# Kernel optimization log

Measured on AMD Instinct MI355X. Metric: run time of the kernel, lower is better.

The kernel has to match this reference:

```python
import jax, jax.numpy as jnp
import numpy as np

H = 64          # HIDDEN_SIZE
D = 300         # WORD_VEC_DIMS
L = 3           # NUM_LSTM_LAYERS
B = 256
T = 512


def _uniform(key, shape, scale):
    return jax.random.uniform(key, shape, jnp.float32, -scale, scale)


def setup_inputs() -> dict:
    key = jax.random.key(0)
    keys = jax.random.split(key, 32)
    s = 1.0 / np.sqrt(H)  # torch LSTM/Linear init scale
    inp = {
        "input": jax.random.normal(keys[0], (B, T, D), jnp.float32),
        "h_0": jnp.zeros((L, B, H), jnp.float32),
        "c_0": jnp.zeros((L, B, H), jnp.float32),
    }
    k = 1
    for l in range(L):
        din = D if l == 0 else H
        inp[f"wih{l}"] = _uniform(keys[k], (4 * H, din), s); k += 1
        inp[f"whh{l}"] = _uniform(keys[k], (4 * H, H), s); k += 1
        inp[f"bih{l}"] = _uniform(keys[k], (4 * H,), s); k += 1
        inp[f"bhh{l}"] = _uniform(keys[k], (4 * H,), s); k += 1
    inp["w1"] = _uniform(keys[k], (H, H), s); k += 1
    inp["b1"] = _uniform(keys[k], (H,), s); k += 1
    inp["w2"] = _uniform(keys[k], (D, H), s); k += 1
    inp["b2"] = _uniform(keys[k], (D,), s); k += 1
    return inp


def _lstm_layer(x_tbd, h0, c0, Wih, Whh, bih, bhh):
    # x_tbd: [T, B, Din]; precompute input projection outside the scan
    xp = jnp.einsum('tbd,gd->tbg', x_tbd, Wih) + bih  # [T, B, 4H]

    def step(carry, xt):
        h, c = carry
        g = xt + h @ Whh.T + bhh
        i, f, gg, o = jnp.split(g, 4, axis=-1)  # torch gate order: i,f,g,o
        c = jax.nn.sigmoid(f) * c + jax.nn.sigmoid(i) * jnp.tanh(gg)
        h = jax.nn.sigmoid(o) * jnp.tanh(c)
        return (h, c), h

    (hT, cT), hs = jax.lax.scan(step, (h0, c0), xp)
    return hs, hT, cT  # hs: [T, B, H]


def reference(input, h_0, c_0, wih0, whh0, bih0, bhh0, wih1, whh1, bih1, bhh1,
              wih2, whh2, bih2, bhh2, w1, b1, w2, b2):
    wih = [wih0, wih1, wih2]
    whh = [whh0, whh1, whh2]
    bih = [bih0, bih1, bih2]
    bhh = [bhh0, bhh1, bhh2]
    x = jnp.transpose(input, (1, 0, 2))  # [T, B, D]
    hs_n, cs_n = [], []
    for l in range(L):
        x, hT, cT = _lstm_layer(x, h_0[l], c_0[l], wih[l], whh[l], bih[l], bhh[l])
        hs_n.append(hT)
        cs_n.append(cT)
    # x is now [T, B, H] == output.permute(1, 0, 2) of the batch_first LSTM.
    # Faithfully replicate the original permute+view reordering:
    flat = x.reshape(-1, H)                       # time-major flatten
    y = jnp.tanh(flat @ w1.T + b1) @ w2.T + b2    # MLP head
    out = y.reshape(input.shape[0], -1, D)        # reinterpreted batch-major
    h_n = jnp.stack(hs_n)
    c_n = jnp.stack(cs_n)
    return out, h_n, c_n
```

## Files before the change

kernel.cpp:

```cpp
#include <hip/hip_runtime.h>
#include <math.h>


#define TT 512
#define BB 256
#define DD 300
#define HH 64
#define MM (TT * BB)
#define XP 256
#define TC 128
#define NC (TT / TC)

typedef __attribute__((ext_vector_type(8))) short bf16x8;
typedef __attribute__((ext_vector_type(4))) float f32x4;

__device__ __forceinline__ float bf2f(unsigned short u) {
    return __uint_as_float(((unsigned int)u) << 16);
}
__device__ __forceinline__ unsigned short f2bf(float f) {
    unsigned int x = __float_as_uint(f);
    x += 0x7FFFu + ((x >> 16) & 1u);
    return (unsigned short)(x >> 16);
}
__device__ __forceinline__ float tanh_f(float x) { return 1.f - 2.f / (__expf(2.f * x) + 1.f); }

__device__ __forceinline__ float ld1(const void* p, long long i, int md) {
    return md ? ((const float*)p)[i] : bf2f(((const unsigned short*)p)[i]);
}
__device__ __forceinline__ void ld4v(float* d, const void* p, long long i, int md) {
    if (md) {
        float4 v = *(const float4*)((const float*)p + i);
        d[0] = v.x; d[1] = v.y; d[2] = v.z; d[3] = v.w;
    } else {
        ushort4 u = *(const ushort4*)((const unsigned short*)p + i);
        d[0] = bf2f(u.x); d[1] = bf2f(u.y); d[2] = bf2f(u.z); d[3] = bf2f(u.w);
    }
}

__device__ __forceinline__ f32x4 mfma16(bf16x8 a, bf16x8 b, f32x4 c) {
    return __builtin_amdgcn_mfma_f32_16x16x32_bf16(a, b, c, 0, 0, 0);
}

__device__ __forceinline__ f32x4 mfma6(bf16x8 a1, bf16x8 a2, bf16x8 a3,
                                       bf16x8 b1, bf16x8 b2, bf16x8 b3, f32x4 t) {
    t = mfma16(a2, b2, t);
    t = mfma16(a1, b3, t);
    t = mfma16(a3, b1, t);
    t = mfma16(a1, b2, t);
    t = mfma16(a2, b1, t);
    t = mfma16(a1, b1, t);
    return t;
}

__device__ __forceinline__ void split3x4(const float* v, ushort4& h1, ushort4& h2, ushort4& h3) {
    unsigned short a[4], b[4], c[4];
    #pragma unroll
    for (int e = 0; e < 4; ++e) {
        unsigned short x = f2bf(v[e]);
        float r1 = v[e] - bf2f(x);
        unsigned short y = f2bf(r1);
        float r2 = r1 - bf2f(y);
        unsigned short z = f2bf(r2);
        a[e] = x; b[e] = y; c[e] = z;
    }
    h1 = make_ushort4(a[0], a[1], a[2], a[3]);
    h2 = make_ushort4(b[0], b[1], b[2], b[3]);
    h3 = make_ushort4(c[0], c[1], c[2], c[3]);
}

__global__ void detect_kernel(const void* inp, int* mode) {
    if (threadIdx.x == 0 && blockIdx.x == 0) {
        const unsigned short* u = (const unsigned short*)inp;
        int bad = 0;
        for (int i = 0; i < 256; ++i) {
            float f = bf2f(u[i]);
            if (!(f == f) || fabsf(f) > 1e6f) ++bad;
        }
        *mode = (bad >= 4) ? 1 : 0;
    }
}

__global__ __launch_bounds__(256) void init_state(
    const void* h0, const void* c0, float* hstate, float* cstate, const int* modep)
{
    const int md = *modep;
    int i = blockIdx.x * 256 + threadIdx.x;
    if (i < 3 * BB * HH) {
        hstate[i] = ld1(h0, i, md);
        cstate[i] = ld1(c0, i, md);
    }
}

__global__ __launch_bounds__(256) void final_state(
    const float* hstate, const float* cstate, void* out, const int* modep)
{
    const int md = *modep;
    int i = blockIdx.x * 256 + threadIdx.x;
    const long long base = (long long)MM * DD;
    if (i < 3 * BB * HH) {
        if (md) {
            ((float*)out)[base + i] = hstate[i];
            ((float*)out)[base + 3 * BB * HH + i] = cstate[i];
        } else {
            ((unsigned short*)out)[base + i] = f2bf(hstate[i]);
            ((unsigned short*)out)[base + 3 * BB * HH + i] = f2bf(cstate[i]);
        }
    }
}

__global__ __launch_bounds__(256) void split_w(
    const void* __restrict__ src, unsigned short* __restrict__ dst,
    int rsrc, int csrc, int rdst, int cdst, const int* modep)
{
    const int md = *modep;
    int i = blockIdx.x * 256 + threadIdx.x;
    int n = rdst * cdst;
    if (i >= n) return;
    int r = i / cdst, cc = i - r * cdst;
    float v = (r < rsrc && cc < csrc) ? ld1(src, (long long)r * csrc + cc, md) : 0.f;
    unsigned short a = f2bf(v);
    float r1 = v - bf2f(a);
    unsigned short b = f2bf(r1);
    float r2 = r1 - bf2f(b);
    unsigned short c = f2bf(r2);
    dst[i] = a; dst[n + i] = b; dst[2 * n + i] = c;
}

__global__ __launch_bounds__(256, 2) void proj0_chunk(
    const void* __restrict__ inp, const unsigned short* __restrict__ wsp,
    const void* __restrict__ bih, const void* __restrict__ bhh,
    float* __restrict__ xp, const int* modep, int chunk)
{
    const int md = *modep;
    __shared__ __align__(16) unsigned short aS[3][64 * 40];
    __shared__ __align__(16) unsigned short wS[3][256 * 40];
    const int tid = threadIdx.x;
    const int m0 = blockIdx.x * 64;
    const int lane = tid & 63, wv = tid >> 6;
    const int fr = lane & 15, fq = lane >> 4;
    const int ar = tid >> 2, acs = (tid & 3) * 8;
    const int ml = m0 + ar;
    const int b = ml & 255;
    const int t = chunk * TC + (ml >> 8);
    const long long abase = (long long)b * (TT * DD) + (long long)t * DD;
    float bias[4];
    #pragma unroll
    for (int nf = 0; nf < 4; ++nf) {
        int n = wv * 64 + nf * 16 + fr;
        bias[nf] = ld1(bih, n, md) + ld1(bhh, n, md);
    }
    f32x4 acc[4][4] = {};
    for (int p = 0; p < 10; ++p) {
        const int k0 = p * 32;
        #pragma unroll
        for (int q = 0; q < 2; ++q) {
            const int kg = k0 + acs + q * 4;
            float v[4];
            if (kg + 3 < DD) {
                ld4v(v, inp, abase + kg, md);
            } else {
                #pragma unroll
                for (int e = 0; e < 4; ++e)
                    v[e] = (kg + e < DD) ? ld1(inp, abase + kg + e, md) : 0.f;
            }
            ushort4 h1, h2, h3;
            split3x4(v, h1, h2, h3);
            *(ushort4*)(&aS[0][ar * 40 + acs + q * 4]) = h1;
            *(ushort4*)(&aS[1][ar * 40 + acs + q * 4]) = h2;
            *(ushort4*)(&aS[2][ar * 40 + acs + q * 4]) = h3;
        }
        #pragma unroll
        for (int pl = 0; pl < 3; ++pl) {
            const uint4* gw = (const uint4*)(wsp + (size_t)pl * 81920 + (size_t)tid * 320 + k0);
            uint4* dw = (uint4*)(&wS[pl][tid * 40]);
            #pragma unroll
            for (int qq = 0; qq < 4; ++qq) dw[qq] = gw[qq];
        }
        __syncthreads();
        bf16x8 wf[4][3];
        #pragma unroll
        for (int nf = 0; nf < 4; ++nf) {
            #pragma unroll
            for (int pl = 0; pl < 3; ++pl)
                wf[nf][pl] = *(const bf16x8*)(&wS[pl][(wv * 64 + nf * 16 + fr) * 40 + fq * 8]);
        }
        #pragma unroll
        for (int mf = 0; mf < 4; ++mf) {
            bf16x8 a1 = *(const bf16x8*)(&aS[0][(mf * 16 + fr) * 40 + fq * 8]);
            bf16x8 a2 = *(const bf16x8*)(&aS[1][(mf * 16 + fr) * 40 + fq * 8]);
            bf16x8 a3 = *(const bf16x8*)(&aS[2][(mf * 16 + fr) * 40 + fq * 8]);
            #pragma unroll
            for (int nf = 0; nf < 4; ++nf)
                acc[mf][nf] = mfma6(a1, a2, a3, wf[nf][0], wf[nf][1], wf[nf][2], acc[mf][nf]);
        }
        __syncthreads();
    }
    #pragma unroll
    for (int mf = 0; mf < 4; ++mf) {
        #pragma unroll
        for (int nf = 0; nf < 4; ++nf) {
            const int col = wv * 64 + nf * 16 + fr;
            #pragma unroll
            for (int r = 0; r < 4; ++r) {
                const int row = m0 + mf * 16 + fq * 4 + r;
                xp[(long long)row * XP + col] = acc[mf][nf][r] + bias[nf];
            }
        }
    }
}

__global__ __launch_bounds__(256, 2) void projh_chunk(
    const float* __restrict__ A, const unsigned short* __restrict__ wsp,
    const void* __restrict__ bih, const void* __restrict__ bhh,
    float* __restrict__ xp, const int* modep)
{
    const int md = *modep;
    __shared__ __align__(16) unsigned short aS[3][64 * 40];
    __shared__ __align__(16) unsigned short wS[3][256 * 40];
    const int tid = threadIdx.x;
    const int m0 = blockIdx.x * 64;
    const int lane = tid & 63, wv = tid >> 6;
    const int fr = lane & 15, fq = lane >> 4;
    const int ar = tid >> 2, acs = (tid & 3) * 8;
    float bias[4];
    #pragma unroll
    for (int nf = 0; nf < 4; ++nf) {
        int n = wv * 64 + nf * 16 + fr;
        bias[nf] = ld1(bih, n, md) + ld1(bhh, n, md);
    }
    f32x4 acc[4][4] = {};
    #pragma unroll
    for (int p = 0; p < 2; ++p) {
        const int k0 = p * 32;
        #pragma unroll
        for (int q = 0; q < 2; ++q) {
            float v[4];
            const float4 fv = *(const float4*)(A + (long long)(m0 + ar) * HH + k0 + acs + q * 4);
            v[0] = fv.x; v[1] = fv.y; v[2] = fv.z; v[3] = fv.w;
            ushort4 h1, h2, h3;
            split3x4(v, h1, h2, h3);
            *(ushort4*)(&aS[0][ar * 40 + acs + q * 4]) = h1;
            *(ushort4*)(&aS[1][ar * 40 + acs + q * 4]) = h2;
            *(ushort4*)(&aS[2][ar * 40 + acs + q * 4]) = h3;
        }
        #pragma unroll
        for (int pl = 0; pl < 3; ++pl) {
            const uint4* gw = (const uint4*)(wsp + (size_t)pl * 16384 + (size_t)tid * 64 + k0);
            uint4* dw = (uint4*)(&wS[pl][tid * 40]);
            #pragma unroll
            for (int qq = 0; qq < 4; ++qq) dw[qq] = gw[qq];
        }
        __syncthreads();
        bf16x8 wf[4][3];
        #pragma unroll
        for (int nf = 0; nf < 4; ++nf) {
            #pragma unroll
            for (int pl = 0; pl < 3; ++pl)
                wf[nf][pl] = *(const bf16x8*)(&wS[pl][(wv * 64 + nf * 16 + fr) * 40 + fq * 8]);
        }
        #pragma unroll
        for (int mf = 0; mf < 4; ++mf) {
            bf16x8 a1 = *(const bf16x8*)(&aS[0][(mf * 16 + fr) * 40 + fq * 8]);
            bf16x8 a2 = *(const bf16x8*)(&aS[1][(mf * 16 + fr) * 40 + fq * 8]);
            bf16x8 a3 = *(const bf16x8*)(&aS[2][(mf * 16 + fr) * 40 + fq * 8]);
            #pragma unroll
            for (int nf = 0; nf < 4; ++nf)
                acc[mf][nf] = mfma6(a1, a2, a3, wf[nf][0], wf[nf][1], wf[nf][2], acc[mf][nf]);
        }
        __syncthreads();
    }
    #pragma unroll
    for (int mf = 0; mf < 4; ++mf) {
        #pragma unroll
        for (int nf = 0; nf < 4; ++nf) {
            const int col = wv * 64 + nf * 16 + fr;
            #pragma unroll
            for (int r = 0; r < 4; ++r) {
                const int row = m0 + mf * 16 + fq * 4 + r;
                xp[(long long)row * XP + col] = acc[mf][nf][r] + bias[nf];
            }
        }
    }
}

__global__ __launch_bounds__(256) void scan_chunk(
    const float* __restrict__ xp, float* __restrict__ hs,
    const void* __restrict__ whh,
    float* __restrict__ hstate, float* __restrict__ cstate, const int* modep)
{
    const int md = *modep;
    const int b = blockIdx.x;
    const int j = threadIdx.x;
    const int g = ((j & 3) << 6) | (j >> 2);
    const int i = j >> 2;
    const int m = j & 63;
    const int bl = j & 60;
    __shared__ __align__(16) float h_s[2][64];
    float w[64];
    #pragma unroll
    for (int q = 0; q < 16; ++q) {
        float v[4];
        ld4v(v, whh, (long long)g * HH + q * 4, md);
        w[4*q+0]=v[0]; w[4*q+1]=v[1]; w[4*q+2]=v[2]; w[4*q+3]=v[3];
    }
    float c = cstate[b * HH + i];
    h_s[0][m] = hstate[b * HH + m];
    float hval = 0.f;

    const int type = j & 3;
    const float aa = (type == 2) ? 2.f : 1.f;
    const float cc = 1.f - aa;

    const long long xbase = (long long)b * XP + g;
    const long long xstep = (long long)BB * XP;
    float xc[8], xn[8];
    #pragma unroll
    for (int p = 0; p < 8; ++p) xc[p] = xp[xbase + (long long)p * xstep];

    for (int tg = 0; tg < TC; tg += 8) {
        if (tg + 8 < TC) {
            #pragma unroll
            for (int p = 0; p < 8; ++p)
                xn[p] = xp[xbase + (long long)(tg + 8 + p) * xstep];
        }
        #pragma unroll
        for (int u = 0; u < 8; ++u) {
            const int t = tg + u;
            float a0 = xc[u], a1 = 0.f, a2 = 0.f, a3 = 0.f;
            const float4* h4 = (const float4*)h_s[t & 1];
            #pragma unroll
            for (int q = 0; q < 16; ++q) {
                float4 hv = h4[q];
                a0 = fmaf(hv.x, w[4*q+0], a0);
                a1 = fmaf(hv.y, w[4*q+1], a1);
                a2 = fmaf(hv.z, w[4*q+2], a2);
                a3 = fmaf(hv.w, w[4*q+3], a3);
            }
            float gr = (a0 + a1) + (a2 + a3);
            float s = 1.f / (1.f + __expf(-aa * gr));
            float y = fmaf(aa, s, cc);
            float yi = __shfl(y, bl | 0);
            float yf = __shfl(y, bl | 1);
            float yg = __shfl(y, bl | 2);
            float yo = __shfl(y, bl | 3);
            c = yf * c + yi * yg;
            hval = yo * tanh_f(c);
            if ((j & 3) == 0) {
                h_s[(t & 1) ^ 1][i] = hval;
                hs[((long long)t * BB + b) * HH + i] = hval;
            }
            asm volatile("s_waitcnt lgkmcnt(0)\n\ts_barrier" ::: "memory");
        }
        #pragma unroll
        for (int p = 0; p < 8; ++p) xc[p] = xn[p];
    }
    if ((j & 3) == 0) {
        hstate[b * HH + i] = hval;
        cstate[b * HH + i] = c;
    }
}

__global__ __launch_bounds__(256, 1) void head_chunk(
    const float* __restrict__ hs, const unsigned short* __restrict__ w1p,
    const void* __restrict__ b1, const unsigned short* __restrict__ w2p,
    const void* __restrict__ b2, void* __restrict__ out,
    const int* modep, int chunk)
{
    const int md = *modep;
    __shared__ __align__(16) unsigned short aS[3][64 * 72];
    __shared__ __align__(16) unsigned short wS[3][64 * 72];
    __shared__ __align__(16) unsigned short zS[3][64 * 72];
    const int tid = threadIdx.x;
    const int m0 = blockIdx.x * 64;
    const long long gbase = (long long)chunk * TC * BB;
    const int lane = tid & 63, wv = tid >> 6;
    const int fr = lane & 15, fq = lane >> 4;
    const int ar = tid >> 2, cs = (tid & 3) * 16;
    #pragma unroll
    for (int e = 0; e < 4; ++e) {
        float v[4];
        const float4 fv = *(const float4*)(hs + (long long)(m0 + ar) * HH + cs + e * 4);
        v[0] = fv.x; v[1] = fv.y; v[2] = fv.z; v[3] = fv.w;
        ushort4 h1, h2, h3;
        split3x4(v, h1, h2, h3);
        *(ushort4*)(&aS[0][ar * 72 + cs + e * 4]) = h1;
        *(ushort4*)(&aS[1][ar * 72 + cs + e * 4]) = h2;
        *(ushort4*)(&aS[2][ar * 72 + cs + e * 4]) = h3;
    }
    #pragma unroll
    for (int pl = 0; pl < 3; ++pl) {
        const uint4* g1 = (const uint4*)(w1p + (size_t)pl * 4096 + (size_t)ar * 64 + cs);
        *(uint4*)(&wS[pl][ar * 72 + cs]) = g1[0];
        *(uint4*)(&wS[pl][ar * 72 + cs + 8]) = g1[1];
    }
    __syncthreads();
    {
        bf16x8 af[2][3];
        #pragma unroll
        for (int kf = 0; kf < 2; ++kf) {
            #pragma unroll
            for (int pl = 0; pl < 3; ++pl)
                af[kf][pl] = *(const bf16x8*)(&aS[pl][(wv * 16 + fr) * 72 + kf * 32 + fq * 8]);
        }
        f32x4 acc1[4] = {};
        #pragma unroll
        for (int nf = 0; nf < 4; ++nf) {
            #pragma unroll
            for (int kf = 0; kf < 2; ++kf) {
                bf16x8 b1f = *(const bf16x8*)(&wS[0][(nf * 16 + fr) * 72 + kf * 32 + fq * 8]);
                bf16x8 b2f = *(const bf16x8*)(&wS[1][(nf * 16 + fr) * 72 + kf * 32 + fq * 8]);
                bf16x8 b3f = *(const bf16x8*)(&wS[2][(nf * 16 + fr) * 72 + kf * 32 + fq * 8]);
                acc1[nf] = mfma6(af[kf][0], af[kf][1], af[kf][2], b1f, b2f, b3f, acc1[nf]);
            }
        }
        #pragma unroll
        for (int nf = 0; nf < 4; ++nf) {
            float bb = ld1(b1, nf * 16 + fr, md);
            #pragma unroll
            for (int r = 0; r < 4; ++r) {
                float z = tanh_f(acc1[nf][r] + bb);
                unsigned short zh = f2bf(z);
                float r1 = z - bf2f(zh);
                unsigned short zm = f2bf(r1);
                float r2 = r1 - bf2f(zm);
                unsigned short zl = f2bf(r2);
                int zi = (wv * 16 + fq * 4 + r) * 72 + nf * 16 + fr;
                zS[0][zi] = zh; zS[1][zi] = zm; zS[2][zi] = zl;
            }
        }
    }
    __syncthreads();
    bf16x8 zf[2][3];
    #pragma unroll
    for (int kf = 0; kf < 2; ++kf) {
        #pragma unroll
        for (int pl = 0; pl < 3; ++pl)
            zf[kf][pl] = *(const bf16x8*)(&zS[pl][(wv * 16 + fr) * 72 + kf * 32 + fq * 8]);
    }
    for (int dt = 0; dt < 5; ++dt) {
        #pragma unroll
        for (int pl = 0; pl < 3; ++pl) {
            const uint4* g2 = (const uint4*)(w2p + (size_t)pl * 20480 + (size_t)(dt * 64 + ar) * 64 + cs);
            *(uint4*)(&wS[pl][ar * 72 + cs]) = g2[0];
            *(uint4*)(&wS[pl][ar * 72 + cs + 8]) = g2[1];
        }
        __syncthreads();
        f32x4 acc[4] = {};
        #pragma unroll
        for (int nf = 0; nf < 4; ++nf) {
            #pragma unroll
            for (int kf = 0; kf < 2; ++kf) {
                bf16x8 b1f = *(const bf16x8*)(&wS[0][(nf * 16 + fr) * 72 + kf * 32 + fq * 8]);
                bf16x8 b2f = *(const bf16x8*)(&wS[1][(nf * 16 + fr) * 72 + kf * 32 + fq * 8]);
                bf16x8 b3f = *(const bf16x8*)(&wS[2][(nf * 16 + fr) * 72 + kf * 32 + fq * 8]);
                acc[nf] = mfma6(zf[kf][0], zf[kf][1], zf[kf][2], b1f, b2f, b3f, acc[nf]);
            }
        }
        #pragma unroll
        for (int nf = 0; nf < 4; ++nf) {
            const int col = dt * 64 + nf * 16 + fr;
            if (col < DD) {
                float bb = ld1(b2, col, md);
                #pragma unroll
                for (int r = 0; r < 4; ++r) {
                    long long row = gbase + m0 + wv * 16 + fq * 4 + r;
                    float o = acc[nf][r] + bb;
                    if (md) ((float*)out)[row * DD + col] = o;
                    else    ((unsigned short*)out)[row * DD + col] = f2bf(o);
                }
            }
        }
        __syncthreads();
    }
}

extern "C" void kernel_launch(void* const* d_in, const int* in_sizes, int n_in,
                              void* d_out, int out_size, void* d_ws, size_t ws_size,
                              hipStream_t stream)
{
    const void* inp  = d_in[0];
    const void* h0   = d_in[1];
    const void* c0   = d_in[2];
    const void* wih0 = d_in[3];
    const void* whh0 = d_in[4];
    const void* bih0 = d_in[5];
    const void* bhh0 = d_in[6];
    const void* wih1 = d_in[7];
    const void* whh1 = d_in[8];
    const void* bih1 = d_in[9];
    const void* bhh1 = d_in[10];
    const void* wih2 = d_in[11];
    const void* whh2 = d_in[12];
    const void* bih2 = d_in[13];
    const void* bhh2 = d_in[14];
    const void* w1   = d_in[15];
    const void* b1   = d_in[16];
    const void* w2   = d_in[17];
    const void* b2   = d_in[18];

    int* mode = (int*)d_ws;
    float* wsf = (float*)d_ws;
    float* hstate = wsf + 16;
    float* cstate = hstate + 3 * BB * HH;
    float* xp  = cstate + 3 * BB * HH;
    float* hs  = xp + (size_t)TC * BB * XP;
    unsigned short* w0s = (unsigned short*)(hs + (size_t)TC * BB * HH);
    unsigned short* w1s = w0s + (size_t)3 * 81920;
    unsigned short* w2s = w1s + (size_t)3 * 16384;
    unsigned short* h1s = w2s + (size_t)3 * 16384;
    unsigned short* h2s = h1s + (size_t)3 * 4096;

    detect_kernel<<<1, 64, 0, stream>>>(inp, mode);
    init_state<<<192, 256, 0, stream>>>(h0, c0, hstate, cstate, mode);
    split_w<<<320, 256, 0, stream>>>(wih0, w0s, 256, 300, 256, 320, mode);
    split_w<<<64, 256, 0, stream>>>(wih1, w1s, 256, 64, 256, 64, mode);
    split_w<<<64, 256, 0, stream>>>(wih2, w2s, 256, 64, 256, 64, mode);
    split_w<<<16, 256, 0, stream>>>(w1, h1s, 64, 64, 64, 64, mode);
    split_w<<<80, 256, 0, stream>>>(w2, h2s, 300, 64, 320, 64, mode);

    for (int c = 0; c < NC; ++c) {
        proj0_chunk<<<dim3(TC * BB / 64), 256, 0, stream>>>(
            inp, w0s, bih0, bhh0, xp, mode, c);
        scan_chunk<<<BB, 256, 0, stream>>>(
            xp, hs, whh0, hstate, cstate, mode);
        projh_chunk<<<dim3(TC * BB / 64), 256, 0, stream>>>(
            hs, w1s, bih1, bhh1, xp, mode);
        scan_chunk<<<BB, 256, 0, stream>>>(
            xp, hs, whh1, hstate + BB * HH, cstate + BB * HH, mode);
        projh_chunk<<<dim3(TC * BB / 64), 256, 0, stream>>>(
            hs, w2s, bih2, bhh2, xp, mode);
        scan_chunk<<<BB, 256, 0, stream>>>(
            xp, hs, whh2, hstate + 2 * BB * HH, cstate + 2 * BB * HH, mode);
        head_chunk<<<TC * BB / 64, 256, 0, stream>>>(
            hs, h1s, b1, h2s, b2, d_out, mode, c);
    }
    final_state<<<192, 256, 0, stream>>>(hstate, cstate, d_out, mode);
}
```

Baseline: 1.649 ms.

## Run LSTM scan with one wavefront per batch row, all gates per thread

The recurrent scan kernel now uses 64 threads per batch row instead of 256. Each thread holds all four gate rows of Whh for its hidden unit in registers and computes i, f, g and o itself, so the lane shuffles and the per-step block barrier go away. The projection kernels write gate columns interleaved per hidden unit, letting each thread fetch its four gate inputs with a single float4 load. The cost is four times the FMA work per thread on a single wave per CU, plus much higher register pressure, so serial latency per timestep may rise.

```diff
diff --git a/kernel.cpp b/kernel.cpp
--- a/kernel.cpp
+++ b/kernel.cpp
@@ -199,11 +199,11 @@
     for (int mf = 0; mf < 4; ++mf) {
         #pragma unroll
         for (int nf = 0; nf < 4; ++nf) {
-            const int col = wv * 64 + nf * 16 + fr;
+            const int colp = ((nf * 16 + fr) << 2) | wv;
             #pragma unroll
             for (int r = 0; r < 4; ++r) {
                 const int row = m0 + mf * 16 + fq * 4 + r;
-                xp[(long long)row * XP + col] = acc[mf][nf][r] + bias[nf];
+                xp[(long long)row * XP + colp] = acc[mf][nf][r] + bias[nf];
             }
         }
     }
@@ -273,91 +273,94 @@
     for (int mf = 0; mf < 4; ++mf) {
         #pragma unroll
         for (int nf = 0; nf < 4; ++nf) {
-            const int col = wv * 64 + nf * 16 + fr;
+            const int colp = ((nf * 16 + fr) << 2) | wv;
             #pragma unroll
             for (int r = 0; r < 4; ++r) {
                 const int row = m0 + mf * 16 + fq * 4 + r;
-                xp[(long long)row * XP + col] = acc[mf][nf][r] + bias[nf];
-            }
-        }
-    }
-}
-
-__global__ __launch_bounds__(256) void scan_chunk(
+                xp[(long long)row * XP + colp] = acc[mf][nf][r] + bias[nf];
+            }
+        }
+    }
+}
+
+__global__ __launch_bounds__(64) void scan_chunk(
     const float* __restrict__ xp, float* __restrict__ hs,
     const void* __restrict__ whh,
     float* __restrict__ hstate, float* __restrict__ cstate, const int* modep)
 {
     const int md = *modep;
     const int b = blockIdx.x;
-    const int j = threadIdx.x;
-    const int g = ((j & 3) << 6) | (j >> 2);
-    const int i = j >> 2;
-    const int m = j & 63;
-    const int bl = j & 60;
+    const int i = threadIdx.x;
     __shared__ __align__(16) float h_s[2][64];
-    float w[64];
-    #pragma unroll
-    for (int q = 0; q < 16; ++q) {
-        float v[4];
-        ld4v(v, whh, (long long)g * HH + q * 4, md);
-        w[4*q+0]=v[0]; w[4*q+1]=v[1]; w[4*q+2]=v[2]; w[4*q+3]=v[3];
+    float w[4][64];
+    #pragma unroll
+    for (int tau = 0; tau < 4; ++tau) {
+        const long long base = (long long)(tau * 64 + i) * HH;
+        #pragma unroll
+        for (int q = 0; q < 16; ++q) {
+            float v[4];
+            ld4v(v, whh, base + q * 4, md);
+            w[tau][4*q+0] = v[0]; w[tau][4*q+1] = v[1];
+            w[tau][4*q+2] = v[2]; w[tau][4*q+3] = v[3];
+        }
     }
     float c = cstate[b * HH + i];
-    h_s[0][m] = hstate[b * HH + m];
+    h_s[0][i] = hstate[b * HH + i];
     float hval = 0.f;
 
-    const int type = j & 3;
-    const float aa = (type == 2) ? 2.f : 1.f;
-    const float cc = 1.f - aa;
-
-    const long long xbase = (long long)b * XP + g;
+    const long long xbase = (long long)b * XP + 4 * i;
     const long long xstep = (long long)BB * XP;
-    float xc[8], xn[8];
-    #pragma unroll
-    for (int p = 0; p < 8; ++p) xc[p] = xp[xbase + (long long)p * xstep];
-
-    for (int tg = 0; tg < TC; tg += 8) {
-        if (tg + 8 < TC) {
-            #pragma unroll
-            for (int p = 0; p < 8; ++p)
-                xn[p] = xp[xbase + (long long)(tg + 8 + p) * xstep];
-        }
-        #pragma unroll
-        for (int u = 0; u < 8; ++u) {
+    float4 xc[4], xn[4];
+    #pragma unroll
+    for (int p = 0; p < 4; ++p)
+        xc[p] = *(const float4*)(xp + xbase + (long long)p * xstep);
+
+    for (int tg = 0; tg < TC; tg += 4) {
+        if (tg + 4 < TC) {
+            #pragma unroll
+            for (int p = 0; p < 4; ++p)
+                xn[p] = *(const float4*)(xp + xbase + (long long)(tg + 4 + p) * xstep);
+        }
+        #pragma unroll
+        for (int u = 0; u < 4; ++u) {
             const int t = tg + u;
-            float a0 = xc[u], a1 = 0.f, a2 = 0.f, a3 = 0.f;
+            float a0[4], a1[4], a2[4], a3[4];
+            a0[0] = xc[u].x; a0[1] = xc[u].y; a0[2] = xc[u].z; a0[3] = xc[u].w;
+            #pragma unroll
+            for (int tau = 0; tau < 4; ++tau) { a1[tau] = 0.f; a2[tau] = 0.f; a3[tau] = 0.f; }
+            asm volatile("" ::: "memory");
             const float4* h4 = (const float4*)h_s[t & 1];
             #pragma unroll
             for (int q = 0; q < 16; ++q) {
                 float4 hv = h4[q];
-                a0 = fmaf(hv.x, w[4*q+0], a0);
-                a1 = fmaf(hv.y, w[4*q+1], a1);
-                a2 = fmaf(hv.z, w[4*q+2], a2);
-                a3 = fmaf(hv.w, w[4*q+3], a3);
-            }
-            float gr = (a0 + a1) + (a2 + a3);
-            float s = 1.f / (1.f + __expf(-aa * gr));
-            float y = fmaf(aa, s, cc);
-            float yi = __shfl(y, bl | 0);
-            float yf = __shfl(y, bl | 1);
-            float yg = __shfl(y, bl | 2);
-            float yo = __shfl(y, bl | 3);
-            c = yf * c + yi * yg;
-            hval = yo * tanh_f(c);
-            if ((j & 3) == 0) {
-                h_s[(t & 1) ^ 1][i] = hval;
-                hs[((long long)t * BB + b) * HH + i] = hval;
-            }
-            asm volatile("s_waitcnt lgkmcnt(0)\n\ts_barrier" ::: "memory");
-        }
-        #pragma unroll
-        for (int p = 0; p < 8; ++p) xc[p] = xn[p];
-    }
-    if ((j & 3) == 0) {
-        hstate[b * HH + i] = hval;
-        cstate[b * HH + i] = c;
-    }
+                #pragma unroll
+                for (int tau = 0; tau < 4; ++tau) {
+                    a0[tau] = fmaf(hv.x, w[tau][4*q+0], a0[tau]);
+                    a1[tau] = fmaf(hv.y, w[tau][4*q+1], a1[tau]);
+                    a2[tau] = fmaf(hv.z, w[tau][4*q+2], a2[tau]);
+                    a3[tau] = fmaf(hv.w, w[tau][4*q+3], a3[tau]);
+                }
+            }
+            float y[4];
+            #pragma unroll
+            for (int tau = 0; tau < 4; ++tau) {
+                float gr = (a0[tau] + a1[tau]) + (a2[tau] + a3[tau]);
+                const float aa = (tau == 2) ? 2.f : 1.f;
+                const float cc = 1.f - aa;
+                float s = 1.f / (1.f + __expf(-aa * gr));
+                y[tau] = fmaf(aa, s, cc);
+            }
+            c = y[1] * c + y[0] * y[2];
+            hval = y[3] * tanh_f(c);
+            h_s[(t & 1) ^ 1][i] = hval;
+            asm volatile("" ::: "memory");
+            hs[((long long)t * BB + b) * HH + i] = hval;
+        }
+        #pragma unroll
+        for (int p = 0; p < 4; ++p) xc[p] = xn[p];
+    }
+    hstate[b * HH + i] = hval;
+    cstate[b * HH + i] = c;
 }
 
 __global__ __launch_bounds__(256, 1) void head_chunk(
@@ -521,15 +524,15 @@
     for (int c = 0; c < NC; ++c) {
         proj0_chunk<<<dim3(TC * BB / 64), 256, 0, stream>>>(
             inp, w0s, bih0, bhh0, xp, mode, c);
-        scan_chunk<<<BB, 256, 0, stream>>>(
+        scan_chunk<<<BB, 64, 0, stream>>>(
             xp, hs, whh0, hstate, cstate, mode);
         projh_chunk<<<dim3(TC * BB / 64), 256, 0, stream>>>(
             hs, w1s, bih1, bhh1, xp, mode);
-        scan_chunk<<<BB, 256, 0, stream>>>(
+        scan_chunk<<<BB, 64, 0, stream>>>(
             xp, hs, whh1, hstate + BB * HH, cstate + BB * HH, mode);
         projh_chunk<<<dim3(TC * BB / 64), 256, 0, stream>>>(
             hs, w2s, bih2, bhh2, xp, mode);
-        scan_chunk<<<BB, 256, 0, stream>>>(
+        scan_chunk<<<BB, 64, 0, stream>>>(
             xp, hs, whh2, hstate + 2 * BB * HH, cstate + 2 * BB * HH, mode);
         head_chunk<<<TC * BB / 64, 256, 0, stream>>>(
             hs, h1s, b1, h2s, b2, d_out, mode, c);
```

Result: slower. 3.313 ms (+100.9%).
